# Kernel tuning notes

Hardware: AMD Instinct MI355X
Metric: run time of the kernel (lower is better)

The kernel has to match this reference:

```python
import jax, jax.numpy as jnp
import numpy as np

FUSION_RATIO = 0.1


def graph_conv(src, dst, x, W, b, n):
    # DGL GraphConv, norm='both': h = D_in^{-1/2} A D_out^{-1/2} (x W) + b
    ones = jnp.ones((src.shape[0],), x.dtype)
    deg_out = jnp.clip(jax.ops.segment_sum(ones, src, num_segments=n), 1.0)
    deg_in = jnp.clip(jax.ops.segment_sum(ones, dst, num_segments=n), 1.0)
    h = (x @ W) * (deg_out ** -0.5)[:, None]
    agg = jax.ops.segment_sum(h[src], dst, num_segments=n)  # [n, out]
    return agg * (deg_in ** -0.5)[:, None] + b


def norm_embed(e):
    # z-score (unbiased std, matching torch.std) then min-max
    e = (e - e.mean()) / jnp.std(e, ddof=1)
    return (e - e.min()) / (e.max() - e.min())


def setup_inputs() -> dict:
    key = jax.random.key(0)
    ks = jax.random.split(key, 24)
    n_apig, n_fcg = 50000, 100000
    e_apig, e_fcg = 800000, 1600000
    apig_dim, fcg_dim, hidden, united, ncls = 256, 128, 128, 64, 10
    s = 0.05
    inp = {
        'apig_feat': jax.random.normal(ks[0], (n_apig, apig_dim), jnp.float32),
        'fcg_feat': jax.random.normal(ks[1], (n_fcg, fcg_dim), jnp.float32),
        'W_a1': jax.random.normal(ks[2], (apig_dim, hidden), jnp.float32) * s,
        'b_a1': jnp.zeros((hidden,), jnp.float32),
        'W_a2': jax.random.normal(ks[3], (hidden, hidden), jnp.float32) * s,
        'b_a2': jnp.zeros((hidden,), jnp.float32),
        'W_f1': jax.random.normal(ks[4], (fcg_dim, hidden), jnp.float32) * s,
        'b_f1': jnp.zeros((hidden,), jnp.float32),
        'W_f2': jax.random.normal(ks[5], (hidden, hidden), jnp.float32) * s,
        'b_f2': jnp.zeros((hidden,), jnp.float32),
        'W1': jax.random.normal(ks[6], (hidden, united), jnp.float32) * s,
        'b1': jnp.zeros((united,), jnp.float32),
        'W2': jax.random.normal(ks[7], (united, hidden), jnp.float32) * s,
        'b2': jnp.zeros((hidden,), jnp.float32),
        'W_attn': jax.random.normal(ks[8], (hidden, 1), jnp.float32) * s,
        'b_attn': jnp.zeros((1,), jnp.float32),
        'W_cls': jax.random.normal(ks[9], (hidden, ncls), jnp.float32) * s,
        'b_cls': jnp.zeros((ncls,), jnp.float32),
        'apig_src': jax.random.randint(ks[10], (e_apig,), 0, n_apig, jnp.int32),
        'apig_dst': jax.random.randint(ks[11], (e_apig,), 0, n_apig, jnp.int32),
        'fcg_src': jax.random.randint(ks[12], (e_fcg,), 0, n_fcg, jnp.int32),
        'fcg_dst': jax.random.randint(ks[13], (e_fcg,), 0, n_fcg, jnp.int32),
        'n_apig': n_apig,
        'n_fcg': n_fcg,
    }
    return inp


def reference(apig_feat, fcg_feat, W_a1, b_a1, W_a2, b_a2, W_f1, b_f1, W_f2, b_f2,
              W1, b1, W2, b2, W_attn, b_attn, W_cls, b_cls,
              apig_src, apig_dst, fcg_src, fcg_dst, n_apig, n_fcg):
    h_a1 = jax.nn.relu(graph_conv(apig_src, apig_dst, apig_feat, W_a1, b_a1, n_apig))
    h_f1 = jax.nn.relu(graph_conv(fcg_src, fcg_dst, fcg_feat, W_f1, b_f1, n_fcg))
    a_enc = h_a1 @ W1 + b1
    f_enc = h_f1 @ W1 + b1
    a_sum = a_enc.sum(axis=0)
    f_sum = f_enc.sum(axis=0)
    a_enc = a_enc + FUSION_RATIO * f_sum
    f_enc = f_enc + FUSION_RATIO * a_sum
    a_dec = a_enc @ W2 + b2
    f_dec = f_enc @ W2 + b2
    h_a2 = jax.nn.relu(graph_conv(apig_src, apig_dst, a_dec, W_a2, b_a2, n_apig))
    h_f2 = jax.nn.relu(graph_conv(fcg_src, fcg_dst, f_dec, W_f2, b_f2, n_fcg))
    apig_emb = h_a2.mean(axis=0)  # dgl.mean_nodes, single graph -> [hidden]
    fcg_emb = h_f2.max(axis=0)    # dgl.max_nodes -> [hidden]
    a = norm_embed(apig_emb)
    f = norm_embed(fcg_emb)
    wa = jax.nn.softmax(a @ W_attn + b_attn, axis=0)  # [1] -> 1.0
    wf = jax.nn.softmax(f @ W_attn + b_attn, axis=0)
    emb = a * wa + f * wf
    # dropout is identity at inference
    return emb @ W_cls + b_cls
```

## Files before the change

### kernel.cpp

```cpp
#include <hip/hip_runtime.h>
#include <math.h>


typedef __attribute__((ext_vector_type(8))) short bf16x8;
typedef __attribute__((ext_vector_type(8))) unsigned short u16x8;
typedef __attribute__((ext_vector_type(4))) float f32x4;

#define SORT_T 4096

static __device__ inline unsigned short f2bf(float f) {
  unsigned u = __float_as_uint(f);
  unsigned r = (u + 0x7fff + ((u >> 16) & 1)) >> 16;
  return (unsigned short)r;
}
static __device__ inline float bf2f(unsigned short h) {
  return __uint_as_float(((unsigned)h) << 16);
}

static __device__ inline void scan512(int* x) {
  for (int o = 1; o < 512; o <<= 1) {
    int i0 = threadIdx.x, i1 = threadIdx.x + 256;
    int v0 = (i0 >= o) ? x[i0 - o] : 0;
    int v1 = (i1 >= o) ? x[i1 - o] : 0;
    __syncthreads();
    x[i0] += v0;
    x[i1] += v1;
    __syncthreads();
  }
}

__global__ __launch_bounds__(256) void prep_init_kernel(
    const float* __restrict__ W_a1, const float* __restrict__ W_f1,
    const float* __restrict__ W_a2, const float* __restrict__ W_f2,
    const float* __restrict__ W1, const float* __restrict__ W2,
    unsigned short* __restrict__ T_a1, unsigned short* __restrict__ T_f1,
    unsigned short* __restrict__ T_a2, unsigned short* __restrict__ T_f2,
    unsigned short* __restrict__ T1, unsigned short* __restrict__ T2,
    float* __restrict__ s0, float* __restrict__ s1, int ns,
    float* __restrict__ ea, unsigned* __restrict__ ef, int ne,
    int* __restrict__ offs_a, int* __restrict__ offs_src_a, int n_a, int e_a,
    int* __restrict__ offs_f, int* __restrict__ offs_src_f, int n_f, int e_f) {
  if (blockIdx.x == 0 && blockIdx.y == 0) {
    int i = threadIdx.x;
    if (i < ns) { s0[i] = 0.f; s1[i] = 0.f; }
    if (i < ne) { ea[i] = 0.f; ef[i] = 0u; }
    if (i == 0) {
      offs_a[n_a] = e_a;
      offs_src_a[n_a] = e_a;
      offs_f[n_f] = e_f;
      offs_src_f[n_f] = e_f;
    }
  }
  const float* src;
  unsigned short* dst;
  int K, N;
  switch (blockIdx.y) {
    case 0: src = W_a1; dst = T_a1; K = 256; N = 128; break;
    case 1: src = W_f1; dst = T_f1; K = 128; N = 128; break;
    case 2: src = W_a2; dst = T_a2; K = 128; N = 128; break;
    case 3: src = W_f2; dst = T_f2; K = 128; N = 128; break;
    case 4: src = W1;   dst = T1;   K = 128; N = 64;  break;
    default: src = W2;  dst = T2;   K = 64;  N = 128; break;
  }
  int total = K * N;
  for (int idx = blockIdx.x * 256 + threadIdx.x; idx < total; idx += gridDim.x * 256) {
    int n = idx / K, k = idx - n * K;
    dst[idx] = f2bf(src[(size_t)k * N + n]);
  }
}

__global__ __launch_bounds__(256) void hist2_kernel(
    const int* __restrict__ a_dst, const int* __restrict__ f_dst,
    const int* __restrict__ a_src, const int* __restrict__ f_src,
    int e_a, int E, int* __restrict__ blkhistD, int* __restrict__ blkhistS, int B) {
  __shared__ int hD[512], hS[512];
  for (int i = threadIdx.x; i < 512; i += 256) { hD[i] = 0; hS[i] = 0; }
  __syncthreads();
  int base = blockIdx.x * SORT_T;
  int end = base + SORT_T;
  if (end > E) end = E;
  for (int i = base + threadIdx.x; i < end; i += 256) {
    int kD = (i < e_a) ? a_dst[i] : (f_dst[i - e_a] + 65536);
    int kS = (i < e_a) ? a_src[i] : (f_src[i - e_a] + 65536);
    atomicAdd(&hD[kD >> 9], 1);
    atomicAdd(&hS[kS >> 9], 1);
  }
  __syncthreads();
  for (int i = threadIdx.x; i < 512; i += 256) {
    blkhistD[i * B + blockIdx.x] = hD[i];
    blkhistS[i * B + blockIdx.x] = hS[i];
  }
}

__global__ __launch_bounds__(256) void cursor2_kernel(
    int* __restrict__ blkhistD, int* __restrict__ blkhistS, int B,
    int* __restrict__ bintotalD, int* __restrict__ bintotalS) {
  __shared__ int part[256];
  int isD = blockIdx.x < 512;
  int bin = isD ? blockIdx.x : blockIdx.x - 512;
  int* row = (isD ? blkhistD : blkhistS) + (size_t)bin * B;
  int C = (B + 255) / 256;
  int start = threadIdx.x * C;
  int end = start + C;
  if (end > B) end = B;
  int v[8];
  int s = 0;
  for (int j = start; j < end; ++j) {
    v[j - start] = row[j];
    s += v[j - start];
  }
  part[threadIdx.x] = s;
  __syncthreads();
  for (int o = 1; o < 256; o <<= 1) {
    int u = (threadIdx.x >= o) ? part[threadIdx.x - o] : 0;
    __syncthreads();
    part[threadIdx.x] += u;
    __syncthreads();
  }
  int run = part[threadIdx.x] - s;
  for (int j = start; j < end; ++j) {
    row[j] = run;
    run += v[j - start];
  }
  if (threadIdx.x == 255) (isD ? bintotalD : bintotalS)[bin] = part[255];
}

__global__ __launch_bounds__(256) void scatter2_kernel(
    const int* __restrict__ a_dst, const int* __restrict__ f_dst,
    const int* __restrict__ a_src, const int* __restrict__ f_src,
    int e_a, int E, const int* __restrict__ blkhistD, const int* __restrict__ blkhistS,
    int B, const int* __restrict__ bintotalD, const int* __restrict__ bintotalS,
    int* __restrict__ opack, unsigned short* __restrict__ okey) {
  __shared__ int curD[512], curS[512], tmp[512];
  int b = blockIdx.x, tid = threadIdx.x;
  tmp[tid] = bintotalD[tid];
  tmp[tid + 256] = bintotalD[tid + 256];
  __syncthreads();
  scan512(tmp);
  curD[tid] = tmp[tid] - bintotalD[tid] + blkhistD[tid * B + b];
  curD[tid + 256] = tmp[tid + 256] - bintotalD[tid + 256] + blkhistD[(tid + 256) * B + b];
  __syncthreads();
  tmp[tid] = bintotalS[tid];
  tmp[tid + 256] = bintotalS[tid + 256];
  __syncthreads();
  scan512(tmp);
  curS[tid] = tmp[tid] - bintotalS[tid] + blkhistS[tid * B + b];
  curS[tid + 256] = tmp[tid + 256] - bintotalS[tid + 256] + blkhistS[(tid + 256) * B + b];
  __syncthreads();
  int base = b * SORT_T;
  int end = base + SORT_T;
  if (end > E) end = E;
  for (int i = base + tid; i < end; i += 256) {
    int sv = (i < e_a) ? a_src[i] : f_src[i - e_a];
    int kD = (i < e_a) ? a_dst[i] : (f_dst[i - e_a] + 65536);
    int kS = (i < e_a) ? sv : (sv + 65536);
    int posD = atomicAdd(&curD[kD >> 9], 1);
    opack[posD] = ((kD & 511) << 17) | sv;
    int posS = atomicAdd(&curS[kS >> 9], 1);
    okey[posS] = (unsigned short)(kS & 511);
  }
}

__global__ __launch_bounds__(256) void bucket2_kernel(
    const int* __restrict__ kp, const unsigned short* __restrict__ ks,
    const int* __restrict__ bintotalD, const int* __restrict__ bintotalS,
    int E, int e_a,
    int* __restrict__ csr, int* __restrict__ offs_a, int n_a,
    int* __restrict__ offs_f, int n_f,
    int* __restrict__ offs_src_a, int* __restrict__ offs_src_f) {
  __shared__ int sh0[512], sh1[512], sh2[512];
  int tid = threadIdx.x;
  int isD = blockIdx.x < 512;
  int b = isD ? blockIdx.x : blockIdx.x - 512;
  const int* bt = isD ? bintotalD : bintotalS;
  sh0[tid] = bt[tid];
  sh0[tid + 256] = bt[tid + 256];
  __syncthreads();
  scan512(sh0);
  int e = sh0[b];
  int s = e - bt[b];
  sh1[tid] = 0;
  sh1[tid + 256] = 0;
  __syncthreads();
  if (isD) {
    for (int i = s + tid; i < e; i += 256) atomicAdd(&sh1[kp[i] >> 17], 1);
  } else {
    for (int i = s + tid; i < e; i += 256) atomicAdd(&sh1[ks[i]], 1);
  }
  __syncthreads();
  sh2[tid] = sh1[tid];
  sh2[tid + 256] = sh1[tid + 256];
  __syncthreads();
  scan512(sh2);
  for (int low = tid; low < 512; low += 256) {
    int gpos = s + sh2[low] - sh1[low];
    int key = (b << 9) | low;
    if (isD) {
      sh0[low] = gpos;
      if (key < 65536) {
        if (key < n_a) offs_a[key] = gpos;
      } else {
        int v = key - 65536;
        if (v < n_f) offs_f[v] = gpos - e_a;
      }
    } else {
      if (key < 65536) {
        if (key < n_a) offs_src_a[key] = gpos;
      } else {
        int v = key - 65536;
        if (v < n_f) offs_src_f[v] = gpos - e_a;
      }
    }
  }
  if (isD) {
    __syncthreads();
    for (int i = s + tid; i < e; i += 256) {
      int pv = kp[i];
      int pos = atomicAdd(&sh0[pv >> 17], 1);
      csr[pos] = pv & 0x1FFFF;
    }
  }
}

__global__ void isr_kernel(const int* __restrict__ offs_a, const int* __restrict__ offs_src_a,
                           float* __restrict__ io_a, float* __restrict__ ii_a, int n_a,
                           const int* __restrict__ offs_f, const int* __restrict__ offs_src_f,
                           float* __restrict__ io_f, float* __restrict__ ii_f, int n_f) {
  int i = blockIdx.x * blockDim.x + threadIdx.x;
  if (i < n_a) {
    int ci = offs_a[i + 1] - offs_a[i];
    int co = offs_src_a[i + 1] - offs_src_a[i];
    ii_a[i] = 1.0f / sqrtf((float)(ci < 1 ? 1 : ci));
    io_a[i] = 1.0f / sqrtf((float)(co < 1 ? 1 : co));
  }
  if (i < n_f) {
    int ci = offs_f[i + 1] - offs_f[i];
    int co = offs_src_f[i + 1] - offs_src_f[i];
    ii_f[i] = 1.0f / sqrtf((float)(ci < 1 ? 1 : ci));
    io_f[i] = 1.0f / sqrtf((float)(co < 1 ? 1 : co));
  }
}

template <int K, int N, int INBF16, int ADDV>
static __device__ inline void gemm_body(
    const void* __restrict__ A, const unsigned short* __restrict__ Bt,
    unsigned short* __restrict__ C, int M, int bid,
    const float* __restrict__ add_vec, float add_scale,
    const float* __restrict__ rowscale, const float* __restrict__ bias,
    unsigned short* Bs) {
  constexpr int KS = (K < 128) ? K : 128;
  constexpr int KP = KS + 8;
  constexpr int NT = N / 16;
  constexpr int KK = K / 32;
  constexpr int KKS = KS / 32;
  constexpr int NSTAGE = K / KS;
  constexpr int CHUNKS = (N * KS / 8) / 256;

  const int tid = threadIdx.x;
  const int lane = tid & 63, w = tid >> 6;
  const int q = lane >> 4, l16 = lane & 15;
  const int m0 = bid * 64;
  const int m = m0 + w * 16 + l16;
  const int mload = (m < M) ? m : (M - 1);

  bf16x8 af[KK];
  if constexpr (INBF16) {
    const unsigned short* Ar = (const unsigned short*)A + (size_t)mload * K + q * 8;
#pragma unroll
    for (int kk = 0; kk < KK; ++kk)
      af[kk] = *reinterpret_cast<const bf16x8*>(Ar + kk * 32);
  } else {
    const float* Ar = (const float*)A + (size_t)mload * K + q * 8;
    float4 r0[KK], r1[KK];
#pragma unroll
    for (int kk = 0; kk < KK; ++kk) {
      r0[kk] = *reinterpret_cast<const float4*>(Ar + kk * 32);
      r1[kk] = *reinterpret_cast<const float4*>(Ar + kk * 32 + 4);
    }
#pragma unroll
    for (int kk = 0; kk < KK; ++kk) {
      bf16x8 t;
      t[0] = (short)f2bf(r0[kk].x); t[1] = (short)f2bf(r0[kk].y);
      t[2] = (short)f2bf(r0[kk].z); t[3] = (short)f2bf(r0[kk].w);
      t[4] = (short)f2bf(r1[kk].x); t[5] = (short)f2bf(r1[kk].y);
      t[6] = (short)f2bf(r1[kk].z); t[7] = (short)f2bf(r1[kk].w);
      af[kk] = t;
    }
  }
  if constexpr (ADDV) {
#pragma unroll
    for (int kk = 0; kk < KK; ++kk) {
      float4 av0 = *reinterpret_cast<const float4*>(add_vec + kk * 32 + q * 8);
      float4 av1 = *reinterpret_cast<const float4*>(add_vec + kk * 32 + q * 8 + 4);
      u16x8 u = (u16x8)af[kk];
      bf16x8 t;
      t[0] = (short)f2bf(bf2f(u[0]) + add_scale * av0.x);
      t[1] = (short)f2bf(bf2f(u[1]) + add_scale * av0.y);
      t[2] = (short)f2bf(bf2f(u[2]) + add_scale * av0.z);
      t[3] = (short)f2bf(bf2f(u[3]) + add_scale * av0.w);
      t[4] = (short)f2bf(bf2f(u[4]) + add_scale * av1.x);
      t[5] = (short)f2bf(bf2f(u[5]) + add_scale * av1.y);
      t[6] = (short)f2bf(bf2f(u[6]) + add_scale * av1.z);
      t[7] = (short)f2bf(bf2f(u[7]) + add_scale * av1.w);
      af[kk] = t;
    }
  }

  f32x4 acc[NT] = {};
#pragma unroll
  for (int st = 0; st < NSTAGE; ++st) {
    u16x8 breg[CHUNKS];
#pragma unroll
    for (int c = 0; c < CHUNKS; ++c) {
      int idx = c * 256 + tid;
      int n = idx / (KS / 8), kpos = (idx % (KS / 8)) * 8;
      breg[c] = *reinterpret_cast<const u16x8*>(Bt + (size_t)n * K + st * KS + kpos);
    }
    if (st) __syncthreads();
#pragma unroll
    for (int c = 0; c < CHUNKS; ++c) {
      int idx = c * 256 + tid;
      int n = idx / (KS / 8), kpos = (idx % (KS / 8)) * 8;
      *reinterpret_cast<u16x8*>(&Bs[n * KP + kpos]) = breg[c];
    }
    __syncthreads();
#pragma unroll
    for (int kk = 0; kk < KKS; ++kk) {
#pragma unroll
      for (int nt = 0; nt < NT; ++nt) {
        bf16x8 bf =
            *reinterpret_cast<const bf16x8*>(&Bs[(nt * 16 + l16) * KP + kk * 32 + q * 8]);
        acc[nt] =
            __builtin_amdgcn_mfma_f32_16x16x32_bf16(bf, af[st * KKS + kk], acc[nt], 0, 0, 0);
      }
    }
  }

  if (m < M) {
    float rs = rowscale ? rowscale[m] : 1.0f;
#pragma unroll
    for (int nt = 0; nt < NT; ++nt) {
      float4 bv;
      if (bias)
        bv = *reinterpret_cast<const float4*>(bias + nt * 16 + q * 4);
      else
        bv = make_float4(0.f, 0.f, 0.f, 0.f);
      ushort4 st4;
      st4.x = f2bf(fmaf(acc[nt][0], rs, bv.x));
      st4.y = f2bf(fmaf(acc[nt][1], rs, bv.y));
      st4.z = f2bf(fmaf(acc[nt][2], rs, bv.z));
      st4.w = f2bf(fmaf(acc[nt][3], rs, bv.w));
      *reinterpret_cast<ushort4*>(C + (size_t)m * N + nt * 16 + q * 4) = st4;
    }
  }
}

template <int K, int N, int INBF16, int ADDV>
__global__ __launch_bounds__(256) void gemm_bls_kernel(
    const void* __restrict__ A, const unsigned short* __restrict__ Bt,
    unsigned short* __restrict__ C, int M,
    const float* __restrict__ add_vec, float add_scale,
    const float* __restrict__ rowscale, const float* __restrict__ bias) {
  constexpr int KS = (K < 128) ? K : 128;
  __shared__ __align__(16) unsigned short Bs[N * (KS + 8)];
  gemm_body<K, N, INBF16, ADDV>(A, Bt, C, M, blockIdx.x, add_vec, add_scale,
                                rowscale, bias, Bs);
}

template <int K, int N, int INBF16, int ADDV>
__global__ __launch_bounds__(256) void gemm_bls2_kernel(
    const void* __restrict__ A0, const unsigned short* __restrict__ Bt0,
    unsigned short* __restrict__ C0, int M0,
    const void* __restrict__ A1, const unsigned short* __restrict__ Bt1,
    unsigned short* __restrict__ C1, int M1,
    const float* __restrict__ av0, const float* __restrict__ av1, float add_scale,
    const float* __restrict__ rs0, const float* __restrict__ rs1,
    const float* __restrict__ bias, int gblk) {
  constexpr int KS = (K < 128) ? K : 128;
  __shared__ __align__(16) unsigned short Bs[N * (KS + 8)];
  if ((int)blockIdx.x < gblk) {
    gemm_body<K, N, INBF16, ADDV>(A0, Bt0, C0, M0, blockIdx.x, av0, add_scale,
                                  rs0, bias, Bs);
  } else {
    gemm_body<K, N, INBF16, ADDV>(A1, Bt1, C1, M1, blockIdx.x - gblk, av1, add_scale,
                                  rs1, bias, Bs);
  }
}

__global__ __launch_bounds__(256) void agg2_kernel(
    const unsigned short* __restrict__ XW0, const int* __restrict__ offs0,
    const int* __restrict__ csr0, const float* __restrict__ isr0,
    const float* __restrict__ bias0, void* __restrict__ out0, int n0, int mode0,
    const unsigned short* __restrict__ XW1, const int* __restrict__ offs1,
    const int* __restrict__ csr1, const float* __restrict__ isr1,
    const float* __restrict__ bias1, void* __restrict__ out1, int n1, int mode1,
    int nblk0) {
  __shared__ float red[8][128];
  const unsigned short* XW;
  const int *offs, *csr;
  const float *isr_in, *bias;
  void* out;
  int n, mode, bid;
  if ((int)blockIdx.x < nblk0) {
    XW = XW0; offs = offs0; csr = csr0; isr_in = isr0; bias = bias0;
    out = out0; n = n0; mode = mode0; bid = blockIdx.x;
  } else {
    XW = XW1; offs = offs1; csr = csr1; isr_in = isr1; bias = bias1;
    out = out1; n = n1; mode = mode1; bid = blockIdx.x - nblk0;
  }
  int lane = threadIdx.x & 31;
  int g = threadIdx.x >> 5;
  int node = bid * 8 + g;
  float4 o = make_float4(0.f, 0.f, 0.f, 0.f);
  if (node < n) {
    int e0 = offs[node], e1 = offs[node + 1];
    float4 a0 = make_float4(0.f, 0.f, 0.f, 0.f);
    float4 a1 = a0, a2 = a0, a3 = a0;
    int e = e0;
    for (; e + 4 <= e1; e += 4) {
      int s0 = csr[e], s1 = csr[e + 1], s2 = csr[e + 2], s3 = csr[e + 3];
      ushort4 v0 = *reinterpret_cast<const ushort4*>(&XW[(size_t)s0 * 128 + lane * 4]);
      ushort4 v1 = *reinterpret_cast<const ushort4*>(&XW[(size_t)s1 * 128 + lane * 4]);
      ushort4 v2 = *reinterpret_cast<const ushort4*>(&XW[(size_t)s2 * 128 + lane * 4]);
      ushort4 v3 = *reinterpret_cast<const ushort4*>(&XW[(size_t)s3 * 128 + lane * 4]);
      a0.x += bf2f(v0.x); a0.y += bf2f(v0.y); a0.z += bf2f(v0.z); a0.w += bf2f(v0.w);
      a1.x += bf2f(v1.x); a1.y += bf2f(v1.y); a1.z += bf2f(v1.z); a1.w += bf2f(v1.w);
      a2.x += bf2f(v2.x); a2.y += bf2f(v2.y); a2.z += bf2f(v2.z); a2.w += bf2f(v2.w);
      a3.x += bf2f(v3.x); a3.y += bf2f(v3.y); a3.z += bf2f(v3.z); a3.w += bf2f(v3.w);
    }
    for (; e < e1; ++e) {
      int s = csr[e];
      ushort4 v = *reinterpret_cast<const ushort4*>(&XW[(size_t)s * 128 + lane * 4]);
      a0.x += bf2f(v.x); a0.y += bf2f(v.y); a0.z += bf2f(v.z); a0.w += bf2f(v.w);
    }
    float4 acc;
    acc.x = (a0.x + a1.x) + (a2.x + a3.x);
    acc.y = (a0.y + a1.y) + (a2.y + a3.y);
    acc.z = (a0.z + a1.z) + (a2.z + a3.z);
    acc.w = (a0.w + a1.w) + (a2.w + a3.w);
    float sc = isr_in[node];
    float4 b = *reinterpret_cast<const float4*>(&bias[lane * 4]);
    o.x = fmaxf(fmaf(acc.x, sc, b.x), 0.f);
    o.y = fmaxf(fmaf(acc.y, sc, b.y), 0.f);
    o.z = fmaxf(fmaf(acc.z, sc, b.z), 0.f);
    o.w = fmaxf(fmaf(acc.w, sc, b.w), 0.f);
  }
  if (mode == 0) {
    if (node < n) {
      ushort4 st;
      st.x = f2bf(o.x); st.y = f2bf(o.y); st.z = f2bf(o.z); st.w = f2bf(o.w);
      *reinterpret_cast<ushort4*>(&((unsigned short*)out)[(size_t)node * 128 + lane * 4]) = st;
    }
    return;
  }
  red[g][lane * 4 + 0] = o.x;
  red[g][lane * 4 + 1] = o.y;
  red[g][lane * 4 + 2] = o.z;
  red[g][lane * 4 + 3] = o.w;
  __syncthreads();
  if (threadIdx.x < 128) {
    float v = red[0][threadIdx.x];
    if (mode == 1) {
#pragma unroll
      for (int j = 1; j < 8; ++j) v += red[j][threadIdx.x];
    } else {
#pragma unroll
      for (int j = 1; j < 8; ++j) v = fmaxf(v, red[j][threadIdx.x]);
    }
    ((float*)out)[(size_t)bid * 128 + threadIdx.x] = v;
  }
}

__global__ __launch_bounds__(256) void colsum2_kernel(
    const unsigned short* __restrict__ X0, float* __restrict__ out0, int n0,
    const unsigned short* __restrict__ X1, float* __restrict__ out1, int n1,
    int ncol) {
  __shared__ float s[256];
  const unsigned short* X;
  float* out;
  int n, bid;
  if ((int)blockIdx.x < 256) { X = X0; out = out0; n = n0; bid = blockIdx.x; }
  else { X = X1; out = out1; n = n1; bid = blockIdx.x - 256; }
  int col = threadIdx.x % ncol;
  int rpb = 256 / ncol;
  int rb = threadIdx.x / ncol;
  float acc = 0.f;
  for (int r = bid * rpb + rb; r < n; r += 256 * rpb)
    acc += bf2f(X[(size_t)r * ncol + col]);
  s[threadIdx.x] = acc;
  __syncthreads();
  if (threadIdx.x < ncol) {
    float v = 0.f;
    for (int i = 0; i < rpb; ++i) v += s[threadIdx.x + i * ncol];
    atomicAdd(&out[col], v);
  }
}

__global__ __launch_bounds__(256) void colfin_kernel(
    const float* __restrict__ Pa, float* __restrict__ emb_a, int na,
    const float* __restrict__ Pf, unsigned* __restrict__ emb_f, int nf, int ncol) {
  __shared__ float s[256];
  int isSum = blockIdx.x < 256;
  const float* X = isSum ? Pa : Pf;
  int n = isSum ? na : nf;
  int bid = isSum ? blockIdx.x : blockIdx.x - 256;
  int col = threadIdx.x % ncol;
  int rpb = 256 / ncol;
  int rb = threadIdx.x / ncol;
  float acc = 0.f;
  if (isSum) {
    for (int r = bid * rpb + rb; r < n; r += 256 * rpb) acc += X[(size_t)r * ncol + col];
  } else {
    for (int r = bid * rpb + rb; r < n; r += 256 * rpb)
      acc = fmaxf(acc, X[(size_t)r * ncol + col]);
  }
  s[threadIdx.x] = acc;
  __syncthreads();
  if (threadIdx.x < ncol) {
    if (isSum) {
      float v = 0.f;
      for (int i = 0; i < rpb; ++i) v += s[threadIdx.x + i * ncol];
      atomicAdd(&emb_a[col], v);
    } else {
      float v = s[threadIdx.x];
      for (int i = 1; i < rpb; ++i) v = fmaxf(v, s[threadIdx.x + i * ncol]);
      atomicMax(&emb_f[col], __float_as_uint(v));
    }
  }
}

__global__ __launch_bounds__(128) void final_kernel(
    const float* __restrict__ emb_a_sum, const unsigned* __restrict__ emb_f_bits,
    const float* __restrict__ W_cls, const float* __restrict__ b_cls,
    float* __restrict__ out, float inv_n_apig, int ncls) {
  __shared__ float red[128];
  __shared__ float emb[128];
  int t = threadIdx.x;
  float a = emb_a_sum[t] * inv_n_apig;
  float f = __uint_as_float(emb_f_bits[t]);

  float vals[2] = {a, f};
  float norms[2];
#pragma unroll
  for (int which = 0; which < 2; ++which) {
    float x = vals[which];
    red[t] = x;
    __syncthreads();
    for (int o = 64; o > 0; o >>= 1) {
      if (t < o) red[t] += red[t + o];
      __syncthreads();
    }
    float mean = red[0] / 128.f;
    __syncthreads();
    float d = x - mean;
    red[t] = d * d;
    __syncthreads();
    for (int o = 64; o > 0; o >>= 1) {
      if (t < o) red[t] += red[t + o];
      __syncthreads();
    }
    float stdv = sqrtf(red[0] / 127.f);
    __syncthreads();
    float z = d / stdv;
    red[t] = z;
    __syncthreads();
    for (int o = 64; o > 0; o >>= 1) {
      if (t < o) red[t] = fminf(red[t], red[t + o]);
      __syncthreads();
    }
    float zmin = red[0];
    __syncthreads();
    red[t] = z;
    __syncthreads();
    for (int o = 64; o > 0; o >>= 1) {
      if (t < o) red[t] = fmaxf(red[t], red[t + o]);
      __syncthreads();
    }
    float zmax = red[0];
    __syncthreads();
    norms[which] = (z - zmin) / (zmax - zmin);
  }

  emb[t] = norms[0] + norms[1];
  __syncthreads();
  if (t < ncls) {
    float acc = b_cls[t];
    for (int k = 0; k < 128; ++k) acc = fmaf(emb[k], W_cls[k * ncls + t], acc);
    out[t] = acc;
  }
}

extern "C" void kernel_launch(void* const* d_in, const int* in_sizes, int n_in,
                              void* d_out, int out_size, void* d_ws, size_t ws_size,
                              hipStream_t stream) {
  const float* apig_feat = (const float*)d_in[0];
  const float* fcg_feat = (const float*)d_in[1];
  const float* W_a1 = (const float*)d_in[2];
  const float* b_a1 = (const float*)d_in[3];
  const float* W_a2 = (const float*)d_in[4];
  const float* b_a2 = (const float*)d_in[5];
  const float* W_f1 = (const float*)d_in[6];
  const float* b_f1 = (const float*)d_in[7];
  const float* W_f2 = (const float*)d_in[8];
  const float* b_f2 = (const float*)d_in[9];
  const float* W1 = (const float*)d_in[10];
  const float* b1 = (const float*)d_in[11];
  const float* W2 = (const float*)d_in[12];
  const float* b2 = (const float*)d_in[13];
  const float* W_cls = (const float*)d_in[16];
  const float* b_cls = (const float*)d_in[17];
  const int* a_src = (const int*)d_in[18];
  const int* a_dst = (const int*)d_in[19];
  const int* f_src = (const int*)d_in[20];
  const int* f_dst = (const int*)d_in[21];

  const int hidden = in_sizes[3];
  const int united = in_sizes[11];
  const int ncls = in_sizes[17];
  const int apig_dim = in_sizes[2] / hidden;
  const int fcg_dim = in_sizes[6] / hidden;
  const int n_a = in_sizes[0] / apig_dim;
  const int n_f = in_sizes[1] / fcg_dim;
  const int e_a = in_sizes[18];
  const int e_f = in_sizes[20];

  char* w = (char*)d_ws;
  auto alloc = [&](size_t bytes) -> void* {
    void* p = (void*)w;
    w += (bytes + 255) & ~(size_t)255;
    return p;
  };
  const int E_tot = e_a + e_f;
  const int B = (E_tot + SORT_T - 1) / SORT_T;
  const int nblkA = (n_a + 7) / 8, nblkF = (n_f + 7) / 8;

  float* isr_out_a = (float*)alloc((size_t)n_a * 4);
  float* isr_in_a = (float*)alloc((size_t)n_a * 4);
  float* isr_out_f = (float*)alloc((size_t)n_f * 4);
  float* isr_in_f = (float*)alloc((size_t)n_f * 4);
  int* offs_a = (int*)alloc((size_t)(n_a + 1) * 4);
  int* offs_f = (int*)alloc((size_t)(n_f + 1) * 4);
  int* offs_src_a = (int*)alloc((size_t)(n_a + 1) * 4);
  int* offs_src_f = (int*)alloc((size_t)(n_f + 1) * 4);
  int* kp = (int*)alloc((size_t)E_tot * 4);
  unsigned short* okey = (unsigned short*)alloc((size_t)E_tot * 2);
  int* csr = (int*)alloc((size_t)E_tot * 4);
  int* blkhistD = (int*)alloc((size_t)512 * B * 4);
  int* blkhistS = (int*)alloc((size_t)512 * B * 4);
  int* bintotalD = (int*)alloc((size_t)512 * 4);
  int* bintotalS = (int*)alloc((size_t)512 * 4);
  unsigned short* G_a = (unsigned short*)alloc((size_t)n_a * hidden * 2);
  unsigned short* H_a = (unsigned short*)alloc((size_t)n_a * hidden * 2);
  unsigned short* G_f = (unsigned short*)alloc((size_t)n_f * hidden * 2);
  unsigned short* H_f = (unsigned short*)alloc((size_t)n_f * hidden * 2);
  float* P_a = (float*)alloc((size_t)nblkA * hidden * 4);
  float* P_f = (float*)alloc((size_t)nblkF * hidden * 4);
  unsigned short* E_a = G_a;
  unsigned short* E_f = G_f;
  float* a_sum = (float*)alloc((size_t)united * 4);
  float* f_sum = (float*)alloc((size_t)united * 4);
  float* emb_a = (float*)alloc((size_t)hidden * 4);
  unsigned* emb_f = (unsigned*)alloc((size_t)hidden * 4);
  unsigned short* T_a1 = (unsigned short*)alloc((size_t)apig_dim * hidden * 2);
  unsigned short* T_f1 = (unsigned short*)alloc((size_t)fcg_dim * hidden * 2);
  unsigned short* T_a2 = (unsigned short*)alloc((size_t)hidden * hidden * 2);
  unsigned short* T_f2 = (unsigned short*)alloc((size_t)hidden * hidden * 2);
  unsigned short* T1 = (unsigned short*)alloc((size_t)hidden * united * 2);
  unsigned short* T2 = (unsigned short*)alloc((size_t)united * hidden * 2);
  int* csr_a = csr;
  int* csr_f = csr + e_a;
  (void)ws_size;
  (void)n_in;
  (void)out_size;

  dim3 blk(256);

  prep_init_kernel<<<dim3(32, 6), blk, 0, stream>>>(
      W_a1, W_f1, W_a2, W_f2, W1, W2, T_a1, T_f1, T_a2, T_f2, T1, T2,
      a_sum, f_sum, united, emb_a, emb_f, hidden,
      offs_a, offs_src_a, n_a, e_a, offs_f, offs_src_f, n_f, e_f);

  hist2_kernel<<<B, blk, 0, stream>>>(a_dst, f_dst, a_src, f_src, e_a, E_tot,
                                      blkhistD, blkhistS, B);
  cursor2_kernel<<<1024, blk, 0, stream>>>(blkhistD, blkhistS, B, bintotalD, bintotalS);
  scatter2_kernel<<<B, blk, 0, stream>>>(a_dst, f_dst, a_src, f_src, e_a, E_tot,
                                         blkhistD, blkhistS, B, bintotalD, bintotalS,
                                         kp, okey);
  bucket2_kernel<<<1024, blk, 0, stream>>>(kp, okey, bintotalD, bintotalS, E_tot, e_a,
                                           csr, offs_a, n_a, offs_f, n_f,
                                           offs_src_a, offs_src_f);
  isr_kernel<<<(n_f + 255) / 256, blk, 0, stream>>>(offs_a, offs_src_a, isr_out_a, isr_in_a,
                                                    n_a, offs_f, offs_src_f, isr_out_f,
                                                    isr_in_f, n_f);

  const int ga = (n_a + 63) / 64, gf = (n_f + 63) / 64;

  gemm_bls_kernel<256, 128, 0, 0><<<ga, blk, 0, stream>>>(
      apig_feat, T_a1, G_a, n_a, nullptr, 0.f, isr_out_a, nullptr);
  gemm_bls_kernel<128, 128, 0, 0><<<gf, blk, 0, stream>>>(
      fcg_feat, T_f1, G_f, n_f, nullptr, 0.f, isr_out_f, nullptr);
  agg2_kernel<<<nblkA + nblkF, blk, 0, stream>>>(
      G_a, offs_a, csr_a, isr_in_a, b_a1, H_a, n_a, 0,
      G_f, offs_f, csr_f, isr_in_f, b_f1, H_f, n_f, 0, nblkA);
  gemm_bls2_kernel<128, 64, 1, 0><<<ga + gf, blk, 0, stream>>>(
      H_a, T1, E_a, n_a, H_f, T1, E_f, n_f,
      nullptr, nullptr, 0.f, nullptr, nullptr, b1, ga);
  colsum2_kernel<<<512, blk, 0, stream>>>(E_a, a_sum, n_a, E_f, f_sum, n_f, united);
  gemm_bls2_kernel<64, 128, 1, 1><<<ga + gf, blk, 0, stream>>>(
      E_a, T2, H_a, n_a, E_f, T2, H_f, n_f,
      f_sum, a_sum, 0.1f, nullptr, nullptr, b2, ga);
  gemm_bls2_kernel<128, 128, 1, 0><<<ga + gf, blk, 0, stream>>>(
      H_a, T_a2, G_a, n_a, H_f, T_f2, G_f, n_f,
      nullptr, nullptr, 0.f, isr_out_a, isr_out_f, nullptr, ga);
  agg2_kernel<<<nblkA + nblkF, blk, 0, stream>>>(
      G_a, offs_a, csr_a, isr_in_a, b_a2, P_a, n_a, 1,
      G_f, offs_f, csr_f, isr_in_f, b_f2, P_f, n_f, 2, nblkA);
  colfin_kernel<<<512, blk, 0, stream>>>(P_a, emb_a, nblkA, P_f, emb_f, nblkF, hidden);
  final_kernel<<<1, 128, 0, stream>>>(emb_a, emb_f, W_cls, b_cls, (float*)d_out,
                                      1.0f / (float)n_a, ncls);
}
```

Before: 570.7 us.

## Fuse sort stages with first-layer GEMMs and fold degree norms into bucketing

```diff
diff --git a/kernel.cpp b/kernel.cpp
--- a/kernel.cpp
+++ b/kernel.cpp
@@ -29,7 +29,155 @@
   }
 }
 
-__global__ __launch_bounds__(256) void prep_init_kernel(
+template <int K, int N, int INBF16, int ADDV, int CSUM>
+static __device__ inline void gemm_body(
+    const void* __restrict__ A, const unsigned short* __restrict__ Bt,
+    unsigned short* __restrict__ C, int M, int bid,
+    const float* __restrict__ add_vec, float add_scale,
+    const float* __restrict__ rowscale, const float* __restrict__ bias,
+    unsigned short* Bs, float* __restrict__ csum) {
+  constexpr int KS = (K < 128) ? K : 128;
+  constexpr int KP = KS + 8;
+  constexpr int NT = N / 16;
+  constexpr int KK = K / 32;
+  constexpr int KKS = KS / 32;
+  constexpr int NSTAGE = K / KS;
+  constexpr int CHUNKS = (N * KS / 8) / 256;
+
+  const int tid = threadIdx.x;
+  const int lane = tid & 63, w = tid >> 6;
+  const int q = lane >> 4, l16 = lane & 15;
+  const int m0 = bid * 64;
+  const int m = m0 + w * 16 + l16;
+  const int mload = (m < M) ? m : (M - 1);
+
+  bf16x8 af[KK];
+  if constexpr (INBF16) {
+    const unsigned short* Ar = (const unsigned short*)A + (size_t)mload * K + q * 8;
+#pragma unroll
+    for (int kk = 0; kk < KK; ++kk)
+      af[kk] = *reinterpret_cast<const bf16x8*>(Ar + kk * 32);
+  } else {
+    const float* Ar = (const float*)A + (size_t)mload * K + q * 8;
+    float4 r0[KK], r1[KK];
+#pragma unroll
+    for (int kk = 0; kk < KK; ++kk) {
+      r0[kk] = *reinterpret_cast<const float4*>(Ar + kk * 32);
+      r1[kk] = *reinterpret_cast<const float4*>(Ar + kk * 32 + 4);
+    }
+#pragma unroll
+    for (int kk = 0; kk < KK; ++kk) {
+      bf16x8 t;
+      t[0] = (short)f2bf(r0[kk].x); t[1] = (short)f2bf(r0[kk].y);
+      t[2] = (short)f2bf(r0[kk].z); t[3] = (short)f2bf(r0[kk].w);
+      t[4] = (short)f2bf(r1[kk].x); t[5] = (short)f2bf(r1[kk].y);
+      t[6] = (short)f2bf(r1[kk].z); t[7] = (short)f2bf(r1[kk].w);
+      af[kk] = t;
+    }
+  }
+  if constexpr (ADDV) {
+#pragma unroll
+    for (int kk = 0; kk < KK; ++kk) {
+      float4 av0 = *reinterpret_cast<const float4*>(add_vec + kk * 32 + q * 8);
+      float4 av1 = *reinterpret_cast<const float4*>(add_vec + kk * 32 + q * 8 + 4);
+      u16x8 u = (u16x8)af[kk];
+      bf16x8 t;
+      t[0] = (short)f2bf(bf2f(u[0]) + add_scale * av0.x);
+      t[1] = (short)f2bf(bf2f(u[1]) + add_scale * av0.y);
+      t[2] = (short)f2bf(bf2f(u[2]) + add_scale * av0.z);
+      t[3] = (short)f2bf(bf2f(u[3]) + add_scale * av0.w);
+      t[4] = (short)f2bf(bf2f(u[4]) + add_scale * av1.x);
+      t[5] = (short)f2bf(bf2f(u[5]) + add_scale * av1.y);
+      t[6] = (short)f2bf(bf2f(u[6]) + add_scale * av1.z);
+      t[7] = (short)f2bf(bf2f(u[7]) + add_scale * av1.w);
+      af[kk] = t;
+    }
+  }
+
+  f32x4 acc[NT] = {};
+#pragma unroll
+  for (int st = 0; st < NSTAGE; ++st) {
+    u16x8 breg[CHUNKS];
+#pragma unroll
+    for (int c = 0; c < CHUNKS; ++c) {
+      int idx = c * 256 + tid;
+      int n = idx / (KS / 8), kpos = (idx % (KS / 8)) * 8;
+      breg[c] = *reinterpret_cast<const u16x8*>(Bt + (size_t)n * K + st * KS + kpos);
+    }
+    if (st) __syncthreads();
+#pragma unroll
+    for (int c = 0; c < CHUNKS; ++c) {
+      int idx = c * 256 + tid;
+      int n = idx / (KS / 8), kpos = (idx % (KS / 8)) * 8;
+      *reinterpret_cast<u16x8*>(&Bs[n * KP + kpos]) = breg[c];
+    }
+    __syncthreads();
+#pragma unroll
+    for (int kk = 0; kk < KKS; ++kk) {
+#pragma unroll
+      for (int nt = 0; nt < NT; ++nt) {
+        bf16x8 bf =
+            *reinterpret_cast<const bf16x8*>(&Bs[(nt * 16 + l16) * KP + kk * 32 + q * 8]);
+        acc[nt] =
+            __builtin_amdgcn_mfma_f32_16x16x32_bf16(bf, af[st * KKS + kk], acc[nt], 0, 0, 0);
+      }
+    }
+  }
+
+  const bool valid = (m < M);
+  float rs = 1.0f;
+  if (rowscale != nullptr && valid) rs = rowscale[m];
+  float* cs = (float*)Bs;
+  if constexpr (CSUM) {
+    __syncthreads();
+    if (tid < N) cs[tid] = 0.f;
+    __syncthreads();
+  }
+#pragma unroll
+  for (int nt = 0; nt < NT; ++nt) {
+    float4 bv;
+    if (bias)
+      bv = *reinterpret_cast<const float4*>(bias + nt * 16 + q * 4);
+    else
+      bv = make_float4(0.f, 0.f, 0.f, 0.f);
+    float v0 = fmaf(acc[nt][0], rs, bv.x);
+    float v1 = fmaf(acc[nt][1], rs, bv.y);
+    float v2 = fmaf(acc[nt][2], rs, bv.z);
+    float v3 = fmaf(acc[nt][3], rs, bv.w);
+    if (valid) {
+      ushort4 st4;
+      st4.x = f2bf(v0); st4.y = f2bf(v1); st4.z = f2bf(v2); st4.w = f2bf(v3);
+      *reinterpret_cast<ushort4*>(C + (size_t)m * N + nt * 16 + q * 4) = st4;
+    }
+    if constexpr (CSUM) {
+      float t0 = valid ? v0 : 0.f, t1 = valid ? v1 : 0.f;
+      float t2 = valid ? v2 : 0.f, t3 = valid ? v3 : 0.f;
+      t0 += __shfl_xor(t0, 1); t0 += __shfl_xor(t0, 2);
+      t0 += __shfl_xor(t0, 4); t0 += __shfl_xor(t0, 8);
+      t1 += __shfl_xor(t1, 1); t1 += __shfl_xor(t1, 2);
+      t1 += __shfl_xor(t1, 4); t1 += __shfl_xor(t1, 8);
+      t2 += __shfl_xor(t2, 1); t2 += __shfl_xor(t2, 2);
+      t2 += __shfl_xor(t2, 4); t2 += __shfl_xor(t2, 8);
+      t3 += __shfl_xor(t3, 1); t3 += __shfl_xor(t3, 2);
+      t3 += __shfl_xor(t3, 4); t3 += __shfl_xor(t3, 8);
+      if (l16 == 0) {
+        atomicAdd(&cs[nt * 16 + q * 4 + 0], t0);
+        atomicAdd(&cs[nt * 16 + q * 4 + 1], t1);
+        atomicAdd(&cs[nt * 16 + q * 4 + 2], t2);
+        atomicAdd(&cs[nt * 16 + q * 4 + 3], t3);
+      }
+    }
+  }
+  if constexpr (CSUM) {
+    __syncthreads();
+    if (tid < N) atomicAdd(&csum[tid], cs[tid]);
+  }
+}
+
+__global__ __launch_bounds__(256) void histprep_kernel(
+    const int* __restrict__ a_dst, const int* __restrict__ f_dst,
+    const int* __restrict__ a_src, const int* __restrict__ f_src,
+    int e_a, int E, int* __restrict__ blkhistD, int* __restrict__ blkhistS, int B,
     const float* __restrict__ W_a1, const float* __restrict__ W_f1,
     const float* __restrict__ W_a2, const float* __restrict__ W_f2,
     const float* __restrict__ W1, const float* __restrict__ W2,
@@ -38,23 +186,44 @@
     unsigned short* __restrict__ T1, unsigned short* __restrict__ T2,
     float* __restrict__ s0, float* __restrict__ s1, int ns,
     float* __restrict__ ea, unsigned* __restrict__ ef, int ne,
-    int* __restrict__ offs_a, int* __restrict__ offs_src_a, int n_a, int e_a,
-    int* __restrict__ offs_f, int* __restrict__ offs_src_f, int n_f, int e_f) {
-  if (blockIdx.x == 0 && blockIdx.y == 0) {
+    int* __restrict__ offs_a, int n_a, int* __restrict__ offs_f, int n_f,
+    int e_f_rel, int* __restrict__ done_cnt) {
+  __shared__ int hD[512], hS[512];
+  if ((int)blockIdx.x < B) {
+    for (int i = threadIdx.x; i < 512; i += 256) { hD[i] = 0; hS[i] = 0; }
+    __syncthreads();
+    int base = blockIdx.x * SORT_T;
+    int end = base + SORT_T;
+    if (end > E) end = E;
+    for (int i = base + threadIdx.x; i < end; i += 256) {
+      int kD = (i < e_a) ? a_dst[i] : (f_dst[i - e_a] + 65536);
+      int kS = (i < e_a) ? a_src[i] : (f_src[i - e_a] + 65536);
+      atomicAdd(&hD[kD >> 9], 1);
+      atomicAdd(&hS[kS >> 9], 1);
+    }
+    __syncthreads();
+    for (int i = threadIdx.x; i < 512; i += 256) {
+      blkhistD[i * B + blockIdx.x] = hD[i];
+      blkhistS[i * B + blockIdx.x] = hS[i];
+    }
+    return;
+  }
+  int pb = blockIdx.x - B;
+  if (pb == 0) {
     int i = threadIdx.x;
     if (i < ns) { s0[i] = 0.f; s1[i] = 0.f; }
     if (i < ne) { ea[i] = 0.f; ef[i] = 0u; }
     if (i == 0) {
       offs_a[n_a] = e_a;
-      offs_src_a[n_a] = e_a;
-      offs_f[n_f] = e_f;
-      offs_src_f[n_f] = e_f;
-    }
-  }
+      offs_f[n_f] = e_f_rel;
+      *done_cnt = 0;
+    }
+  }
+  int py = pb >> 5, px = pb & 31;
   const float* src;
   unsigned short* dst;
   int K, N;
-  switch (blockIdx.y) {
+  switch (py) {
     case 0: src = W_a1; dst = T_a1; K = 256; N = 128; break;
     case 1: src = W_f1; dst = T_f1; K = 128; N = 128; break;
     case 2: src = W_a2; dst = T_a2; K = 128; N = 128; break;
@@ -63,102 +232,97 @@
     default: src = W2;  dst = T2;   K = 64;  N = 128; break;
   }
   int total = K * N;
-  for (int idx = blockIdx.x * 256 + threadIdx.x; idx < total; idx += gridDim.x * 256) {
+  for (int idx = px * 256 + threadIdx.x; idx < total; idx += 32 * 256) {
     int n = idx / K, k = idx - n * K;
     dst[idx] = f2bf(src[(size_t)k * N + n]);
   }
 }
 
-__global__ __launch_bounds__(256) void hist2_kernel(
-    const int* __restrict__ a_dst, const int* __restrict__ f_dst,
-    const int* __restrict__ a_src, const int* __restrict__ f_src,
-    int e_a, int E, int* __restrict__ blkhistD, int* __restrict__ blkhistS, int B) {
-  __shared__ int hD[512], hS[512];
-  for (int i = threadIdx.x; i < 512; i += 256) { hD[i] = 0; hS[i] = 0; }
-  __syncthreads();
-  int base = blockIdx.x * SORT_T;
-  int end = base + SORT_T;
-  if (end > E) end = E;
-  for (int i = base + threadIdx.x; i < end; i += 256) {
-    int kD = (i < e_a) ? a_dst[i] : (f_dst[i - e_a] + 65536);
-    int kS = (i < e_a) ? a_src[i] : (f_src[i - e_a] + 65536);
-    atomicAdd(&hD[kD >> 9], 1);
-    atomicAdd(&hS[kS >> 9], 1);
-  }
-  __syncthreads();
-  for (int i = threadIdx.x; i < 512; i += 256) {
-    blkhistD[i * B + blockIdx.x] = hD[i];
-    blkhistS[i * B + blockIdx.x] = hS[i];
-  }
-}
-
-__global__ __launch_bounds__(256) void cursor2_kernel(
+__global__ __launch_bounds__(256) void cursor_gemmA_kernel(
     int* __restrict__ blkhistD, int* __restrict__ blkhistS, int B,
-    int* __restrict__ bintotalD, int* __restrict__ bintotalS) {
-  __shared__ int part[256];
-  int isD = blockIdx.x < 512;
-  int bin = isD ? blockIdx.x : blockIdx.x - 512;
-  int* row = (isD ? blkhistD : blkhistS) + (size_t)bin * B;
-  int C = (B + 255) / 256;
-  int start = threadIdx.x * C;
-  int end = start + C;
-  if (end > B) end = B;
-  int v[8];
-  int s = 0;
-  for (int j = start; j < end; ++j) {
-    v[j - start] = row[j];
-    s += v[j - start];
-  }
-  part[threadIdx.x] = s;
-  __syncthreads();
-  for (int o = 1; o < 256; o <<= 1) {
-    int u = (threadIdx.x >= o) ? part[threadIdx.x - o] : 0;
-    __syncthreads();
-    part[threadIdx.x] += u;
-    __syncthreads();
-  }
-  int run = part[threadIdx.x] - s;
-  for (int j = start; j < end; ++j) {
-    row[j] = run;
-    run += v[j - start];
-  }
-  if (threadIdx.x == 255) (isD ? bintotalD : bintotalS)[bin] = part[255];
-}
-
-__global__ __launch_bounds__(256) void scatter2_kernel(
+    int* __restrict__ bintotalD, int* __restrict__ bintotalS,
+    const float* __restrict__ A, const unsigned short* __restrict__ Bt,
+    unsigned short* __restrict__ C, int M) {
+  __shared__ __align__(16) char smem[34816];
+  if (blockIdx.x < 1024) {
+    int* part = (int*)smem;
+    int isD = blockIdx.x < 512;
+    int bin = isD ? blockIdx.x : blockIdx.x - 512;
+    int* row = (isD ? blkhistD : blkhistS) + (size_t)bin * B;
+    int C_ = (B + 255) / 256;
+    int start = threadIdx.x * C_;
+    int end = start + C_;
+    if (end > B) end = B;
+    int v[8];
+    int s = 0;
+    for (int j = start; j < end; ++j) {
+      v[j - start] = row[j];
+      s += v[j - start];
+    }
+    part[threadIdx.x] = s;
+    __syncthreads();
+    for (int o = 1; o < 256; o <<= 1) {
+      int u = (threadIdx.x >= o) ? part[threadIdx.x - o] : 0;
+      __syncthreads();
+      part[threadIdx.x] += u;
+      __syncthreads();
+    }
+    int run = part[threadIdx.x] - s;
+    for (int j = start; j < end; ++j) {
+      row[j] = run;
+      run += v[j - start];
+    }
+    if (threadIdx.x == 255) (isD ? bintotalD : bintotalS)[bin] = part[255];
+    return;
+  }
+  gemm_body<256, 128, 0, 0, 0>(A, Bt, C, M, blockIdx.x - 1024, nullptr, 0.f,
+                               nullptr, nullptr, (unsigned short*)smem, nullptr);
+}
+
+__global__ __launch_bounds__(256) void scatter_gemmF_kernel(
     const int* __restrict__ a_dst, const int* __restrict__ f_dst,
     const int* __restrict__ a_src, const int* __restrict__ f_src,
     int e_a, int E, const int* __restrict__ blkhistD, const int* __restrict__ blkhistS,
     int B, const int* __restrict__ bintotalD, const int* __restrict__ bintotalS,
-    int* __restrict__ opack, unsigned short* __restrict__ okey) {
-  __shared__ int curD[512], curS[512], tmp[512];
-  int b = blockIdx.x, tid = threadIdx.x;
-  tmp[tid] = bintotalD[tid];
-  tmp[tid + 256] = bintotalD[tid + 256];
-  __syncthreads();
-  scan512(tmp);
-  curD[tid] = tmp[tid] - bintotalD[tid] + blkhistD[tid * B + b];
-  curD[tid + 256] = tmp[tid + 256] - bintotalD[tid + 256] + blkhistD[(tid + 256) * B + b];
-  __syncthreads();
-  tmp[tid] = bintotalS[tid];
-  tmp[tid + 256] = bintotalS[tid + 256];
-  __syncthreads();
-  scan512(tmp);
-  curS[tid] = tmp[tid] - bintotalS[tid] + blkhistS[tid * B + b];
-  curS[tid + 256] = tmp[tid + 256] - bintotalS[tid + 256] + blkhistS[(tid + 256) * B + b];
-  __syncthreads();
-  int base = b * SORT_T;
-  int end = base + SORT_T;
-  if (end > E) end = E;
-  for (int i = base + tid; i < end; i += 256) {
-    int sv = (i < e_a) ? a_src[i] : f_src[i - e_a];
-    int kD = (i < e_a) ? a_dst[i] : (f_dst[i - e_a] + 65536);
-    int kS = (i < e_a) ? sv : (sv + 65536);
-    int posD = atomicAdd(&curD[kD >> 9], 1);
-    opack[posD] = ((kD & 511) << 17) | sv;
-    int posS = atomicAdd(&curS[kS >> 9], 1);
-    okey[posS] = (unsigned short)(kS & 511);
-  }
+    int* __restrict__ opack, unsigned short* __restrict__ okey,
+    const float* __restrict__ A, const unsigned short* __restrict__ Bt,
+    unsigned short* __restrict__ C, int M) {
+  __shared__ __align__(16) char smem[34816];
+  if ((int)blockIdx.x < B) {
+    int* curD = (int*)smem;
+    int* curS = curD + 512;
+    int* tmp = curS + 512;
+    int b = blockIdx.x, tid = threadIdx.x;
+    tmp[tid] = bintotalD[tid];
+    tmp[tid + 256] = bintotalD[tid + 256];
+    __syncthreads();
+    scan512(tmp);
+    curD[tid] = tmp[tid] - bintotalD[tid] + blkhistD[tid * B + b];
+    curD[tid + 256] = tmp[tid + 256] - bintotalD[tid + 256] + blkhistD[(tid + 256) * B + b];
+    __syncthreads();
+    tmp[tid] = bintotalS[tid];
+    tmp[tid + 256] = bintotalS[tid + 256];
+    __syncthreads();
+    scan512(tmp);
+    curS[tid] = tmp[tid] - bintotalS[tid] + blkhistS[tid * B + b];
+    curS[tid + 256] = tmp[tid + 256] - bintotalS[tid + 256] + blkhistS[(tid + 256) * B + b];
+    __syncthreads();
+    int base = b * SORT_T;
+    int end = base + SORT_T;
+    if (end > E) end = E;
+    for (int i = base + tid; i < end; i += 256) {
+      int sv = (i < e_a) ? a_src[i] : f_src[i - e_a];
+      int kD = (i < e_a) ? a_dst[i] : (f_dst[i - e_a] + 65536);
+      int kS = (i < e_a) ? sv : (sv + 65536);
+      int posD = atomicAdd(&curD[kD >> 9], 1);
+      opack[posD] = ((kD & 511) << 17) | sv;
+      int posS = atomicAdd(&curS[kS >> 9], 1);
+      okey[posS] = (unsigned short)(kS & 511);
+    }
+    return;
+  }
+  gemm_body<128, 128, 0, 0, 0>(A, Bt, C, M, blockIdx.x - B, nullptr, 0.f,
+                               nullptr, nullptr, (unsigned short*)smem, nullptr);
 }
 
 __global__ __launch_bounds__(256) void bucket2_kernel(
@@ -167,7 +331,8 @@
     int E, int e_a,
     int* __restrict__ csr, int* __restrict__ offs_a, int n_a,
     int* __restrict__ offs_f, int n_f,
-    int* __restrict__ offs_src_a, int* __restrict__ offs_src_f) {
+    float* __restrict__ ii_a, float* __restrict__ ii_f,
+    float* __restrict__ io_a, float* __restrict__ io_f) {
   __shared__ int sh0[512], sh1[512], sh2[512];
   int tid = threadIdx.x;
   int isD = blockIdx.x < 512;
@@ -193,22 +358,24 @@
   __syncthreads();
   scan512(sh2);
   for (int low = tid; low < 512; low += 256) {
-    int gpos = s + sh2[low] - sh1[low];
+    int c = sh1[low];
+    int gpos = s + sh2[low] - c;
     int key = (b << 9) | low;
+    float inv = 1.0f / sqrtf((float)(c < 1 ? 1 : c));
     if (isD) {
       sh0[low] = gpos;
       if (key < 65536) {
-        if (key < n_a) offs_a[key] = gpos;
+        if (key < n_a) { offs_a[key] = gpos; ii_a[key] = inv; }
       } else {
         int v = key - 65536;
-        if (v < n_f) offs_f[v] = gpos - e_a;
+        if (v < n_f) { offs_f[v] = gpos - e_a; ii_f[v] = inv; }
       }
     } else {
       if (key < 65536) {
-        if (key < n_a) offs_src_a[key] = gpos;
+        if (key < n_a) io_a[key] = inv;
       } else {
         int v = key - 65536;
-        if (v < n_f) offs_src_f[v] = gpos - e_a;
+        if (v < n_f) io_f[v] = inv;
       }
     }
   }
@@ -222,152 +389,7 @@
   }
 }
 
-__global__ void isr_kernel(const int* __restrict__ offs_a, const int* __restrict__ offs_src_a,
-                           float* __restrict__ io_a, float* __restrict__ ii_a, int n_a,
-                           const int* __restrict__ offs_f, const int* __restrict__ offs_src_f,
-                           float* __restrict__ io_f, float* __restrict__ ii_f, int n_f) {
-  int i = blockIdx.x * blockDim.x + threadIdx.x;
-  if (i < n_a) {
-    int ci = offs_a[i + 1] - offs_a[i];
-    int co = offs_src_a[i + 1] - offs_src_a[i];
-    ii_a[i] = 1.0f / sqrtf((float)(ci < 1 ? 1 : ci));
-    io_a[i] = 1.0f / sqrtf((float)(co < 1 ? 1 : co));
-  }
-  if (i < n_f) {
-    int ci = offs_f[i + 1] - offs_f[i];
-    int co = offs_src_f[i + 1] - offs_src_f[i];
-    ii_f[i] = 1.0f / sqrtf((float)(ci < 1 ? 1 : ci));
-    io_f[i] = 1.0f / sqrtf((float)(co < 1 ? 1 : co));
-  }
-}
-
-template <int K, int N, int INBF16, int ADDV>
-static __device__ inline void gemm_body(
-    const void* __restrict__ A, const unsigned short* __restrict__ Bt,
-    unsigned short* __restrict__ C, int M, int bid,
-    const float* __restrict__ add_vec, float add_scale,
-    const float* __restrict__ rowscale, const float* __restrict__ bias,
-    unsigned short* Bs) {
-  constexpr int KS = (K < 128) ? K : 128;
-  constexpr int KP = KS + 8;
-  constexpr int NT = N / 16;
-  constexpr int KK = K / 32;
-  constexpr int KKS = KS / 32;
-  constexpr int NSTAGE = K / KS;
-  constexpr int CHUNKS = (N * KS / 8) / 256;
-
-  const int tid = threadIdx.x;
-  const int lane = tid & 63, w = tid >> 6;
-  const int q = lane >> 4, l16 = lane & 15;
-  const int m0 = bid * 64;
-  const int m = m0 + w * 16 + l16;
-  const int mload = (m < M) ? m : (M - 1);
-
-  bf16x8 af[KK];
-  if constexpr (INBF16) {
-    const unsigned short* Ar = (const unsigned short*)A + (size_t)mload * K + q * 8;
-#pragma unroll
-    for (int kk = 0; kk < KK; ++kk)
-      af[kk] = *reinterpret_cast<const bf16x8*>(Ar + kk * 32);
-  } else {
-    const float* Ar = (const float*)A + (size_t)mload * K + q * 8;
-    float4 r0[KK], r1[KK];
-#pragma unroll
-    for (int kk = 0; kk < KK; ++kk) {
-      r0[kk] = *reinterpret_cast<const float4*>(Ar + kk * 32);
-      r1[kk] = *reinterpret_cast<const float4*>(Ar + kk * 32 + 4);
-    }
-#pragma unroll
-    for (int kk = 0; kk < KK; ++kk) {
-      bf16x8 t;
-      t[0] = (short)f2bf(r0[kk].x); t[1] = (short)f2bf(r0[kk].y);
-      t[2] = (short)f2bf(r0[kk].z); t[3] = (short)f2bf(r0[kk].w);
-      t[4] = (short)f2bf(r1[kk].x); t[5] = (short)f2bf(r1[kk].y);
-      t[6] = (short)f2bf(r1[kk].z); t[7] = (short)f2bf(r1[kk].w);
-      af[kk] = t;
-    }
-  }
-  if constexpr (ADDV) {
-#pragma unroll
-    for (int kk = 0; kk < KK; ++kk) {
-      float4 av0 = *reinterpret_cast<const float4*>(add_vec + kk * 32 + q * 8);
-      float4 av1 = *reinterpret_cast<const float4*>(add_vec + kk * 32 + q * 8 + 4);
-      u16x8 u = (u16x8)af[kk];
-      bf16x8 t;
-      t[0] = (short)f2bf(bf2f(u[0]) + add_scale * av0.x);
-      t[1] = (short)f2bf(bf2f(u[1]) + add_scale * av0.y);
-      t[2] = (short)f2bf(bf2f(u[2]) + add_scale * av0.z);
-      t[3] = (short)f2bf(bf2f(u[3]) + add_scale * av0.w);
-      t[4] = (short)f2bf(bf2f(u[4]) + add_scale * av1.x);
-      t[5] = (short)f2bf(bf2f(u[5]) + add_scale * av1.y);
-      t[6] = (short)f2bf(bf2f(u[6]) + add_scale * av1.z);
-      t[7] = (short)f2bf(bf2f(u[7]) + add_scale * av1.w);
-      af[kk] = t;
-    }
-  }
-
-  f32x4 acc[NT] = {};
-#pragma unroll
-  for (int st = 0; st < NSTAGE; ++st) {
-    u16x8 breg[CHUNKS];
-#pragma unroll
-    for (int c = 0; c < CHUNKS; ++c) {
-      int idx = c * 256 + tid;
-      int n = idx / (KS / 8), kpos = (idx % (KS / 8)) * 8;
-      breg[c] = *reinterpret_cast<const u16x8*>(Bt + (size_t)n * K + st * KS + kpos);
-    }
-    if (st) __syncthreads();
-#pragma unroll
-    for (int c = 0; c < CHUNKS; ++c) {
-      int idx = c * 256 + tid;
-      int n = idx / (KS / 8), kpos = (idx % (KS / 8)) * 8;
-      *reinterpret_cast<u16x8*>(&Bs[n * KP + kpos]) = breg[c];
-    }
-    __syncthreads();
-#pragma unroll
-    for (int kk = 0; kk < KKS; ++kk) {
-#pragma unroll
-      for (int nt = 0; nt < NT; ++nt) {
-        bf16x8 bf =
-            *reinterpret_cast<const bf16x8*>(&Bs[(nt * 16 + l16) * KP + kk * 32 + q * 8]);
-        acc[nt] =
-            __builtin_amdgcn_mfma_f32_16x16x32_bf16(bf, af[st * KKS + kk], acc[nt], 0, 0, 0);
-      }
-    }
-  }
-
-  if (m < M) {
-    float rs = rowscale ? rowscale[m] : 1.0f;
-#pragma unroll
-    for (int nt = 0; nt < NT; ++nt) {
-      float4 bv;
-      if (bias)
-        bv = *reinterpret_cast<const float4*>(bias + nt * 16 + q * 4);
-      else
-        bv = make_float4(0.f, 0.f, 0.f, 0.f);
-      ushort4 st4;
-      st4.x = f2bf(fmaf(acc[nt][0], rs, bv.x));
-      st4.y = f2bf(fmaf(acc[nt][1], rs, bv.y));
-      st4.z = f2bf(fmaf(acc[nt][2], rs, bv.z));
-      st4.w = f2bf(fmaf(acc[nt][3], rs, bv.w));
-      *reinterpret_cast<ushort4*>(C + (size_t)m * N + nt * 16 + q * 4) = st4;
-    }
-  }
-}
-
-template <int K, int N, int INBF16, int ADDV>
-__global__ __launch_bounds__(256) void gemm_bls_kernel(
-    const void* __restrict__ A, const unsigned short* __restrict__ Bt,
-    unsigned short* __restrict__ C, int M,
-    const float* __restrict__ add_vec, float add_scale,
-    const float* __restrict__ rowscale, const float* __restrict__ bias) {
-  constexpr int KS = (K < 128) ? K : 128;
-  __shared__ __align__(16) unsigned short Bs[N * (KS + 8)];
-  gemm_body<K, N, INBF16, ADDV>(A, Bt, C, M, blockIdx.x, add_vec, add_scale,
-                                rowscale, bias, Bs);
-}
-
-template <int K, int N, int INBF16, int ADDV>
+template <int K, int N, int INBF16, int ADDV, int CSUM>
 __global__ __launch_bounds__(256) void gemm_bls2_kernel(
     const void* __restrict__ A0, const unsigned short* __restrict__ Bt0,
     unsigned short* __restrict__ C0, int M0,
@@ -375,15 +397,16 @@
     unsigned short* __restrict__ C1, int M1,
     const float* __restrict__ av0, const float* __restrict__ av1, float add_scale,
     const float* __restrict__ rs0, const float* __restrict__ rs1,
-    const float* __restrict__ bias, int gblk) {
+    const float* __restrict__ bias, int gblk,
+    float* __restrict__ cs0, float* __restrict__ cs1) {
   constexpr int KS = (K < 128) ? K : 128;
   __shared__ __align__(16) unsigned short Bs[N * (KS + 8)];
   if ((int)blockIdx.x < gblk) {
-    gemm_body<K, N, INBF16, ADDV>(A0, Bt0, C0, M0, blockIdx.x, av0, add_scale,
-                                  rs0, bias, Bs);
+    gemm_body<K, N, INBF16, ADDV, CSUM>(A0, Bt0, C0, M0, blockIdx.x, av0, add_scale,
+                                        rs0, bias, Bs, cs0);
   } else {
-    gemm_body<K, N, INBF16, ADDV>(A1, Bt1, C1, M1, blockIdx.x - gblk, av1, add_scale,
-                                  rs1, bias, Bs);
+    gemm_body<K, N, INBF16, ADDV, CSUM>(A1, Bt1, C1, M1, blockIdx.x - gblk, av1,
+                                        add_scale, rs1, bias, Bs, cs1);
   }
 }
 
@@ -391,22 +414,23 @@
     const unsigned short* __restrict__ XW0, const int* __restrict__ offs0,
     const int* __restrict__ csr0, const float* __restrict__ isr0,
     const float* __restrict__ bias0, void* __restrict__ out0, int n0, int mode0,
+    const float* __restrict__ io0,
     const unsigned short* __restrict__ XW1, const int* __restrict__ offs1,
     const int* __restrict__ csr1, const float* __restrict__ isr1,
     const float* __restrict__ bias1, void* __restrict__ out1, int n1, int mode1,
-    int nblk0) {
+    const float* __restrict__ io1, int nblk0) {
   __shared__ float red[8][128];
   const unsigned short* XW;
   const int *offs, *csr;
-  const float *isr_in, *bias;
+  const float *isr_in, *bias, *iosrc;
   void* out;
   int n, mode, bid;
   if ((int)blockIdx.x < nblk0) {
     XW = XW0; offs = offs0; csr = csr0; isr_in = isr0; bias = bias0;
-    out = out0; n = n0; mode = mode0; bid = blockIdx.x;
+    out = out0; n = n0; mode = mode0; iosrc = io0; bid = blockIdx.x;
   } else {
     XW = XW1; offs = offs1; csr = csr1; isr_in = isr1; bias = bias1;
-    out = out1; n = n1; mode = mode1; bid = blockIdx.x - nblk0;
+    out = out1; n = n1; mode = mode1; iosrc = io1; bid = blockIdx.x - nblk0;
   }
   int lane = threadIdx.x & 31;
   int g = threadIdx.x >> 5;
@@ -419,19 +443,27 @@
     int e = e0;
     for (; e + 4 <= e1; e += 4) {
       int s0 = csr[e], s1 = csr[e + 1], s2 = csr[e + 2], s3 = csr[e + 3];
+      float w0 = 1.f, w1 = 1.f, w2 = 1.f, w3 = 1.f;
+      if (iosrc) { w0 = iosrc[s0]; w1 = iosrc[s1]; w2 = iosrc[s2]; w3 = iosrc[s3]; }
       ushort4 v0 = *reinterpret_cast<const ushort4*>(&XW[(size_t)s0 * 128 + lane * 4]);
       ushort4 v1 = *reinterpret_cast<const ushort4*>(&XW[(size_t)s1 * 128 + lane * 4]);
       ushort4 v2 = *reinterpret_cast<const ushort4*>(&XW[(size_t)s2 * 128 + lane * 4]);
       ushort4 v3 = *reinterpret_cast<const ushort4*>(&XW[(size_t)s3 * 128 + lane * 4]);
-      a0.x += bf2f(v0.x); a0.y += bf2f(v0.y); a0.z += bf2f(v0.z); a0.w += bf2f(v0.w);
-      a1.x += bf2f(v1.x); a1.y += bf2f(v1.y); a1.z += bf2f(v1.z); a1.w += bf2f(v1.w);
-      a2.x += bf2f(v2.x); a2.y += bf2f(v2.y); a2.z += bf2f(v2.z); a2.w += bf2f(v2.w);
-      a3.x += bf2f(v3.x); a3.y += bf2f(v3.y); a3.z += bf2f(v3.z); a3.w += bf2f(v3.w);
+      a0.x = fmaf(w0, bf2f(v0.x), a0.x); a0.y = fmaf(w0, bf2f(v0.y), a0.y);
+      a0.z = fmaf(w0, bf2f(v0.z), a0.z); a0.w = fmaf(w0, bf2f(v0.w), a0.w);
+      a1.x = fmaf(w1, bf2f(v1.x), a1.x); a1.y = fmaf(w1, bf2f(v1.y), a1.y);
+      a1.z = fmaf(w1, bf2f(v1.z), a1.z); a1.w = fmaf(w1, bf2f(v1.w), a1.w);
+      a2.x = fmaf(w2, bf2f(v2.x), a2.x); a2.y = fmaf(w2, bf2f(v2.y), a2.y);
+      a2.z = fmaf(w2, bf2f(v2.z), a2.z); a2.w = fmaf(w2, bf2f(v2.w), a2.w);
+      a3.x = fmaf(w3, bf2f(v3.x), a3.x); a3.y = fmaf(w3, bf2f(v3.y), a3.y);
+      a3.z = fmaf(w3, bf2f(v3.z), a3.z); a3.w = fmaf(w3, bf2f(v3.w), a3.w);
     }
     for (; e < e1; ++e) {
       int s = csr[e];
+      float w0 = iosrc ? iosrc[s] : 1.f;
       ushort4 v = *reinterpret_cast<const ushort4*>(&XW[(size_t)s * 128 + lane * 4]);
-      a0.x += bf2f(v.x); a0.y += bf2f(v.y); a0.z += bf2f(v.z); a0.w += bf2f(v.w);
+      a0.x = fmaf(w0, bf2f(v.x), a0.x); a0.y = fmaf(w0, bf2f(v.y), a0.y);
+      a0.z = fmaf(w0, bf2f(v.z), a0.z); a0.w = fmaf(w0, bf2f(v.w), a0.w);
     }
     float4 acc;
     acc.x = (a0.x + a1.x) + (a2.x + a3.x);
@@ -471,98 +503,83 @@
   }
 }
 
-__global__ __launch_bounds__(256) void colsum2_kernel(
-    const unsigned short* __restrict__ X0, float* __restrict__ out0, int n0,
-    const unsigned short* __restrict__ X1, float* __restrict__ out1, int n1,
-    int ncol) {
+__global__ __launch_bounds__(256) void colfin_final_kernel(
+    const float* __restrict__ Pa, float* __restrict__ emb_a, int na,
+    const float* __restrict__ Pf, unsigned* __restrict__ emb_f, int nf, int ncol,
+    int* __restrict__ done_cnt, const float* __restrict__ W_cls,
+    const float* __restrict__ b_cls, float* __restrict__ out,
+    float inv_n_apig, int ncls) {
   __shared__ float s[256];
-  const unsigned short* X;
-  float* out;
-  int n, bid;
-  if ((int)blockIdx.x < 256) { X = X0; out = out0; n = n0; bid = blockIdx.x; }
-  else { X = X1; out = out1; n = n1; bid = blockIdx.x - 256; }
-  int col = threadIdx.x % ncol;
-  int rpb = 256 / ncol;
-  int rb = threadIdx.x / ncol;
-  float acc = 0.f;
-  for (int r = bid * rpb + rb; r < n; r += 256 * rpb)
-    acc += bf2f(X[(size_t)r * ncol + col]);
-  s[threadIdx.x] = acc;
+  {
+    int isSum = blockIdx.x < 256;
+    const float* X = isSum ? Pa : Pf;
+    int n = isSum ? na : nf;
+    int bid = isSum ? blockIdx.x : blockIdx.x - 256;
+    int col = threadIdx.x % ncol;
+    int rpb = 256 / ncol;
+    int rb = threadIdx.x / ncol;
+    float acc = 0.f;
+    if (isSum) {
+      for (int r = bid * rpb + rb; r < n; r += 256 * rpb) acc += X[(size_t)r * ncol + col];
+    } else {
+      for (int r = bid * rpb + rb; r < n; r += 256 * rpb)
+        acc = fmaxf(acc, X[(size_t)r * ncol + col]);
+    }
+    s[threadIdx.x] = acc;
+    __syncthreads();
+    if (threadIdx.x < ncol) {
+      if (isSum) {
+        float v = 0.f;
+        for (int i = 0; i < rpb; ++i) v += s[threadIdx.x + i * ncol];
+        atomicAdd(&emb_a[col], v);
+      } else {
+        float v = s[threadIdx.x];
+        for (int i = 1; i < rpb; ++i) v = fmaxf(v, s[threadIdx.x + i * ncol]);
+        atomicMax(&emb_f[col], __float_as_uint(v));
+      }
+    }
+  }
+  __threadfence();
+  __shared__ int lastv;
+  if (threadIdx.x == 0) lastv = (atomicAdd(done_cnt, 1) == 511) ? 1 : 0;
   __syncthreads();
-  if (threadIdx.x < ncol) {
-    float v = 0.f;
-    for (int i = 0; i < rpb; ++i) v += s[threadIdx.x + i * ncol];
-    atomicAdd(&out[col], v);
-  }
-}
-
-__global__ __launch_bounds__(256) void colfin_kernel(
-    const float* __restrict__ Pa, float* __restrict__ emb_a, int na,
-    const float* __restrict__ Pf, unsigned* __restrict__ emb_f, int nf, int ncol) {
-  __shared__ float s[256];
-  int isSum = blockIdx.x < 256;
-  const float* X = isSum ? Pa : Pf;
-  int n = isSum ? na : nf;
-  int bid = isSum ? blockIdx.x : blockIdx.x - 256;
-  int col = threadIdx.x % ncol;
-  int rpb = 256 / ncol;
-  int rb = threadIdx.x / ncol;
-  float acc = 0.f;
-  if (isSum) {
-    for (int r = bid * rpb + rb; r < n; r += 256 * rpb) acc += X[(size_t)r * ncol + col];
-  } else {
-    for (int r = bid * rpb + rb; r < n; r += 256 * rpb)
-      acc = fmaxf(acc, X[(size_t)r * ncol + col]);
-  }
-  s[threadIdx.x] = acc;
-  __syncthreads();
-  if (threadIdx.x < ncol) {
-    if (isSum) {
-      float v = 0.f;
-      for (int i = 0; i < rpb; ++i) v += s[threadIdx.x + i * ncol];
-      atomicAdd(&emb_a[col], v);
-    } else {
-      float v = s[threadIdx.x];
-      for (int i = 1; i < rpb; ++i) v = fmaxf(v, s[threadIdx.x + i * ncol]);
-      atomicMax(&emb_f[col], __float_as_uint(v));
-    }
-  }
-}
-
-__global__ __launch_bounds__(128) void final_kernel(
-    const float* __restrict__ emb_a_sum, const unsigned* __restrict__ emb_f_bits,
-    const float* __restrict__ W_cls, const float* __restrict__ b_cls,
-    float* __restrict__ out, float inv_n_apig, int ncls) {
+  if (!lastv) return;
+
   __shared__ float red[128];
-  __shared__ float emb[128];
+  __shared__ float embs[128];
   int t = threadIdx.x;
-  float a = emb_a_sum[t] * inv_n_apig;
-  float f = __uint_as_float(emb_f_bits[t]);
-
+  float a = 0.f, f = 0.f;
+  if (t < 128) {
+    a = __hip_atomic_load(&emb_a[t], __ATOMIC_RELAXED, __HIP_MEMORY_SCOPE_AGENT) *
+        inv_n_apig;
+    unsigned fb = __hip_atomic_load(&emb_f[t], __ATOMIC_RELAXED, __HIP_MEMORY_SCOPE_AGENT);
+    f = __uint_as_float(fb);
+  }
   float vals[2] = {a, f};
-  float norms[2];
+  float norms[2] = {0.f, 0.f};
 #pragma unroll
   for (int which = 0; which < 2; ++which) {
     float x = vals[which];
-    red[t] = x;
+    __syncthreads();
+    if (t < 128) red[t] = x;
     __syncthreads();
     for (int o = 64; o > 0; o >>= 1) {
       if (t < o) red[t] += red[t + o];
       __syncthreads();
     }
     float mean = red[0] / 128.f;
-    __syncthreads();
     float d = x - mean;
-    red[t] = d * d;
+    __syncthreads();
+    if (t < 128) red[t] = d * d;
     __syncthreads();
     for (int o = 64; o > 0; o >>= 1) {
       if (t < o) red[t] += red[t + o];
       __syncthreads();
     }
     float stdv = sqrtf(red[0] / 127.f);
-    __syncthreads();
     float z = d / stdv;
-    red[t] = z;
+    __syncthreads();
+    if (t < 128) red[t] = z;
     __syncthreads();
     for (int o = 64; o > 0; o >>= 1) {
       if (t < o) red[t] = fminf(red[t], red[t + o]);
@@ -570,22 +587,21 @@
     }
     float zmin = red[0];
     __syncthreads();
-    red[t] = z;
+    if (t < 128) red[t] = z;
     __syncthreads();
     for (int o = 64; o > 0; o >>= 1) {
       if (t < o) red[t] = fmaxf(red[t], red[t + o]);
       __syncthreads();
     }
     float zmax = red[0];
-    __syncthreads();
     norms[which] = (z - zmin) / (zmax - zmin);
   }
-
-  emb[t] = norms[0] + norms[1];
+  __syncthreads();
+  if (t < 128) embs[t] = norms[0] + norms[1];
   __syncthreads();
   if (t < ncls) {
     float acc = b_cls[t];
-    for (int k = 0; k < 128; ++k) acc = fmaf(emb[k], W_cls[k * ncls + t], acc);
+    for (int k = 0; k < 128; ++k) acc = fmaf(embs[k], W_cls[k * ncls + t], acc);
     out[t] = acc;
   }
 }
@@ -640,8 +656,6 @@
   float* isr_in_f = (float*)alloc((size_t)n_f * 4);
   int* offs_a = (int*)alloc((size_t)(n_a + 1) * 4);
   int* offs_f = (int*)alloc((size_t)(n_f + 1) * 4);
-  int* offs_src_a = (int*)alloc((size_t)(n_a + 1) * 4);
-  int* offs_src_f = (int*)alloc((size_t)(n_f + 1) * 4);
   int* kp = (int*)alloc((size_t)E_tot * 4);
   unsigned short* okey = (unsigned short*)alloc((size_t)E_tot * 2);
   int* csr = (int*)alloc((size_t)E_tot * 4);
@@ -661,6 +675,7 @@
   float* f_sum = (float*)alloc((size_t)united * 4);
   float* emb_a = (float*)alloc((size_t)hidden * 4);
   unsigned* emb_f = (unsigned*)alloc((size_t)hidden * 4);
+  int* done_cnt = (int*)alloc(256);
   unsigned short* T_a1 = (unsigned short*)alloc((size_t)apig_dim * hidden * 2);
   unsigned short* T_f1 = (unsigned short*)alloc((size_t)fcg_dim * hidden * 2);
   unsigned short* T_a2 = (unsigned short*)alloc((size_t)hidden * hidden * 2);
@@ -674,48 +689,37 @@
   (void)out_size;
 
   dim3 blk(256);
-
-  prep_init_kernel<<<dim3(32, 6), blk, 0, stream>>>(
+  const int ga = (n_a + 63) / 64, gf = (n_f + 63) / 64;
+
+  histprep_kernel<<<B + 192, blk, 0, stream>>>(
+      a_dst, f_dst, a_src, f_src, e_a, E_tot, blkhistD, blkhistS, B,
       W_a1, W_f1, W_a2, W_f2, W1, W2, T_a1, T_f1, T_a2, T_f2, T1, T2,
       a_sum, f_sum, united, emb_a, emb_f, hidden,
-      offs_a, offs_src_a, n_a, e_a, offs_f, offs_src_f, n_f, e_f);
-
-  hist2_kernel<<<B, blk, 0, stream>>>(a_dst, f_dst, a_src, f_src, e_a, E_tot,
-                                      blkhistD, blkhistS, B);
-  cursor2_kernel<<<1024, blk, 0, stream>>>(blkhistD, blkhistS, B, bintotalD, bintotalS);
-  scatter2_kernel<<<B, blk, 0, stream>>>(a_dst, f_dst, a_src, f_src, e_a, E_tot,
-                                         blkhistD, blkhistS, B, bintotalD, bintotalS,
-                                         kp, okey);
+      offs_a, n_a, offs_f, n_f, e_f, done_cnt);
+  cursor_gemmA_kernel<<<1024 + ga, blk, 0, stream>>>(
+      blkhistD, blkhistS, B, bintotalD, bintotalS, apig_feat, T_a1, G_a, n_a);
+  scatter_gemmF_kernel<<<B + gf, blk, 0, stream>>>(
+      a_dst, f_dst, a_src, f_src, e_a, E_tot, blkhistD, blkhistS, B,
+      bintotalD, bintotalS, kp, okey, fcg_feat, T_f1, G_f, n_f);
   bucket2_kernel<<<1024, blk, 0, stream>>>(kp, okey, bintotalD, bintotalS, E_tot, e_a,
                                            csr, offs_a, n_a, offs_f, n_f,
-                                           offs_src_a, offs_src_f);
-  isr_kernel<<<(n_f + 255) / 256, blk, 0, stream>>>(offs_a, offs_src_a, isr_out_a, isr_in_a,
-                                                    n_a, offs_f, offs_src_f, isr_out_f,
-                                                    isr_in_f, n_f);
-
-  const int ga = (n_a + 63) / 64, gf = (n_f + 63) / 64;
-
-  gemm_bls_kernel<256, 128, 0, 0><<<ga, blk, 0, stream>>>(
-      apig_feat, T_a1, G_a, n_a, nullptr, 0.f, isr_out_a, nullptr);
-  gemm_bls_kernel<128, 128, 0, 0><<<gf, blk, 0, stream>>>(
-      fcg_feat, T_f1, G_f, n_f, nullptr, 0.f, isr_out_f, nullptr);
+                                           isr_in_a, isr_in_f, isr_out_a, isr_out_f);
   agg2_kernel<<<nblkA + nblkF, blk, 0, stream>>>(
-      G_a, offs_a, csr_a, isr_in_a, b_a1, H_a, n_a, 0,
-      G_f, offs_f, csr_f, isr_in_f, b_f1, H_f, n_f, 0, nblkA);
-  gemm_bls2_kernel<128, 64, 1, 0><<<ga + gf, blk, 0, stream>>>(
+      G_a, offs_a, csr_a, isr_in_a, b_a1, H_a, n_a, 0, isr_out_a,
+      G_f, offs_f, csr_f, isr_in_f, b_f1, H_f, n_f, 0, isr_out_f, nblkA);
+  gemm_bls2_kernel<128, 64, 1, 0, 1><<<ga + gf, blk, 0, stream>>>(
       H_a, T1, E_a, n_a, H_f, T1, E_f, n_f,
-      nullptr, nullptr, 0.f, nullptr, nullptr, b1, ga);
-  colsum2_kernel<<<512, blk, 0, stream>>>(E_a, a_sum, n_a, E_f, f_sum, n_f, united);
-  gemm_bls2_kernel<64, 128, 1, 1><<<ga + gf, blk, 0, stream>>>(
+      nullptr, nullptr, 0.f, nullptr, nullptr, b1, ga, a_sum, f_sum);
+  gemm_bls2_kernel<64, 128, 1, 1, 0><<<ga + gf, blk, 0, stream>>>(
       E_a, T2, H_a, n_a, E_f, T2, H_f, n_f,
-      f_sum, a_sum, 0.1f, nullptr, nullptr, b2, ga);
-  gemm_bls2_kernel<128, 128, 1, 0><<<ga + gf, blk, 0, stream>>>(
+      f_sum, a_sum, 0.1f, nullptr, nullptr, b2, ga, nullptr, nullptr);
+  gemm_bls2_kernel<128, 128, 1, 0, 0><<<ga + gf, blk, 0, stream>>>(
       H_a, T_a2, G_a, n_a, H_f, T_f2, G_f, n_f,
-      nullptr, nullptr, 0.f, isr_out_a, isr_out_f, nullptr, ga);
+      nullptr, nullptr, 0.f, isr_out_a, isr_out_f, nullptr, ga, nullptr, nullptr);
   agg2_kernel<<<nblkA + nblkF, blk, 0, stream>>>(
-      G_a, offs_a, csr_a, isr_in_a, b_a2, P_a, n_a, 1,
-      G_f, offs_f, csr_f, isr_in_f, b_f2, P_f, n_f, 2, nblkA);
-  colfin_kernel<<<512, blk, 0, stream>>>(P_a, emb_a, nblkA, P_f, emb_f, nblkF, hidden);
-  final_kernel<<<1, 128, 0, stream>>>(emb_a, emb_f, W_cls, b_cls, (float*)d_out,
-                                      1.0f / (float)n_a, ncls);
-}
+      G_a, offs_a, csr_a, isr_in_a, b_a2, P_a, n_a, 1, nullptr,
+      G_f, offs_f, csr_f, isr_in_f, b_f2, P_f, n_f, 2, nullptr, nblkA);
+  colfin_final_kernel<<<512, blk, 0, stream>>>(
+      P_a, emb_a, nblkA, P_f, emb_f, nblkF, hidden,
+      done_cnt, W_cls, b_cls, (float*)d_out, 1.0f / (float)n_a, ncls);
+}
```

Result: slower. 610.1 us (+6.9%).
